# Kernel optimization log

Hardware: AMD Instinct MI355X
Metric: run time of the kernel (lower is better)

Reference implementation:

```python
import jax, jax.numpy as jnp
import numpy as np
import math

FEATURE_DIM = 512
QK_DIM = 256
EPS = 1e-12  # torch F.normalize eps


def _l2norm(x):
    n = jnp.linalg.norm(x, axis=-1, keepdims=True)
    return x / jnp.maximum(n, EPS)


def setup_inputs() -> dict:
    key = jax.random.key(0)
    ks = jax.random.split(key, 6)
    B, Nq, Nk = 16, 2048, 2048
    query = jax.random.normal(ks[0], (B, Nq, FEATURE_DIM), dtype=jnp.float32)
    key_t = jax.random.normal(ks[1], (B, Nk, FEATURE_DIM // 2), dtype=jnp.float32)
    value = jax.random.normal(ks[2], (B, Nk, FEATURE_DIM // 2), dtype=jnp.float32)
    # weights stored torch-style [out, in], init N(0, sqrt(2/out))
    WQ = jax.random.normal(ks[3], (QK_DIM, FEATURE_DIM), dtype=jnp.float32) * math.sqrt(2.0 / QK_DIM)
    WK = jax.random.normal(ks[4], (QK_DIM, FEATURE_DIM // 2), dtype=jnp.float32) * math.sqrt(2.0 / QK_DIM)
    WV = jax.random.normal(ks[5], (FEATURE_DIM, FEATURE_DIM // 2), dtype=jnp.float32) * math.sqrt(2.0 / FEATURE_DIM)
    return {"query": query, "key": key_t, "value": value, "WQ": WQ, "WK": WK, "WV": WV}


def reference(query, key, value, WQ, WK, WV):
    temp = QK_DIM ** (-0.5)
    w_q = _l2norm(jnp.einsum('bnf,qf->bnq', query, WQ))      # [B, Nq, D]
    w_k = _l2norm(jnp.einsum('bmf,qf->bmq', key, WK))        # [B, Nk, D]
    dot = jnp.einsum('bnd,bmd->bnm', w_q, w_k)               # cosine sims
    affinity = jax.nn.softmax(dot * temp, axis=-1)
    w_v = _l2norm(jnp.einsum('bmf,vf->bmv', value, WV))      # [B, Nk, F]
    out = jnp.einsum('bnm,bmv->bnv', affinity, w_v)
    return out + query
```

## Files before the change

### kernel.cpp

```cpp
#include <hip/hip_runtime.h>

typedef float        f32x4  __attribute__((ext_vector_type(4)));
typedef float        f32x16 __attribute__((ext_vector_type(16)));
typedef unsigned int u32x4  __attribute__((ext_vector_type(4)));
typedef unsigned int u32x2  __attribute__((ext_vector_type(2)));
typedef int          i32x2  __attribute__((ext_vector_type(2)));
typedef __bf16       bf16x8 __attribute__((ext_vector_type(8)));

#define DEVFN static __device__ __forceinline__

DEVFN unsigned cvtpk(float a, float b){
  unsigned r;
  asm("v_cvt_pk_bf16_f32 %0, %1, %2" : "=v"(r) : "v"(a), "v"(b));
  return r;
}
DEVFN float exp2_hw(float x){
  float r;
  asm("v_exp_f32 %0, %1" : "=v"(r) : "v"(x));
  return r;
}
DEVFN bf16x8 as_bf(u32x4 v){ union{u32x4 u; bf16x8 b;} x; x.u=v; return x.b; }

DEVFN unsigned char f2fp8(float v){
  int r = __builtin_amdgcn_cvt_pk_fp8_f32(v, v, 0, false);
  return (unsigned char)(r & 0xff);
}
DEVFN unsigned pk4_fp8(float a, float b, float c, float d){
  int r = __builtin_amdgcn_cvt_pk_fp8_f32(a, b, 0, false);
  r = __builtin_amdgcn_cvt_pk_fp8_f32(c, d, r, true);
  return (unsigned)r;
}
DEVFN long mk64(unsigned lo, unsigned hi){
  return (long)(((unsigned long long)hi << 32) | lo);
}

DEVFN void plswap(unsigned &x, unsigned &y, int h){
#if __has_builtin(__builtin_amdgcn_permlane32_swap)
  i32x2 r = __builtin_amdgcn_permlane32_swap((int)x, (int)y, false, false);
  x = (unsigned)r[0]; y = (unsigned)r[1];
#else
  unsigned ox = (unsigned)__shfl_xor((int)x, 32);
  unsigned oy = (unsigned)__shfl_xor((int)y, 32);
  unsigned nx = h ? oy : x;
  unsigned ny = h ? y  : ox;
  x = nx; y = ny;
#endif
}

DEVFN void gload16(const char* src, char* lds){
  __builtin_amdgcn_global_load_lds(
      (__attribute__((address_space(1))) void*)src,
      (__attribute__((address_space(3))) void*)lds, 16, 0, 0);
}

constexpr int BB = 16, NQ = 2048, NK = 2048, F = 512, D = 256, FV = 512;

template<int KD, int ND, int MODE>
__global__ __launch_bounds__(256,2) void proj_kernel(const float* __restrict__ X,
                                                     const float* __restrict__ W,
                                                     unsigned char* __restrict__ Y,
                                                     float scale)
{
  constexpr bool TR = (MODE == 2);
  constexpr int NW = ND/4;
  constexpr int AF = TR ? 8 : 2;
  constexpr int BF = TR ? 2 : NW/16;
  __shared__ __align__(16) char xsm[32*80];
  __shared__ __align__(16) char wsm[ND*80];
  __shared__ float wsum[4][32];
  const int tid = threadIdx.x;
  const int lane = tid & 63;
  const int wid = tid >> 6;
  const int q16 = lane & 15;
  const int g = lane >> 4;
  const int row0 = blockIdx.x * 32;
  const int rX = tid >> 3, cX = (tid & 7) * 4;

  f32x4 z4 = {0.f,0.f,0.f,0.f};
  f32x4 acc[AF][BF];
  #pragma unroll
  for (int i=0;i<AF;i++){
    #pragma unroll
    for (int j=0;j<BF;j++) acc[i][j] = z4;
  }

  for (int k0 = 0; k0 < KD; k0 += 32){
    {
      f32x4 v = *(const f32x4*)(X + (size_t)(row0+rX)*KD + k0 + cX);
      u32x2 p; p[0]=cvtpk(v[0],v[1]); p[1]=cvtpk(v[2],v[3]);
      *(u32x2*)(xsm + rX*80 + cX*2) = p;
    }
    #pragma unroll
    for (int j=0;j<ND/32;j++){
      int r = j*32 + rX;
      f32x4 v = *(const f32x4*)(W + (size_t)r*KD + k0 + cX);
      u32x2 p; p[0]=cvtpk(v[0],v[1]); p[1]=cvtpk(v[2],v[3]);
      *(u32x2*)(wsm + r*80 + cX*2) = p;
    }
    __syncthreads();
    if constexpr (!TR){
      bf16x8 a[2], bb[BF];
      #pragma unroll
      for (int mi=0;mi<2;mi++)  a[mi]  = as_bf(*(const u32x4*)(xsm + (16*mi+q16)*80 + g*16));
      #pragma unroll
      for (int ni=0;ni<BF;ni++) bb[ni] = as_bf(*(const u32x4*)(wsm + (wid*NW + 16*ni + q16)*80 + g*16));
      #pragma unroll
      for (int mi=0;mi<2;mi++){
        #pragma unroll
        for (int ni=0;ni<BF;ni++)
          acc[mi][ni] = __builtin_amdgcn_mfma_f32_16x16x32_bf16(a[mi], bb[ni], acc[mi][ni], 0,0,0);
      }
    } else {
      bf16x8 a[8], bb[2];
      #pragma unroll
      for (int ai=0;ai<8;ai++) a[ai] = as_bf(*(const u32x4*)(wsm + (wid*NW + 16*ai + q16)*80 + g*16));
      #pragma unroll
      for (int ci=0;ci<2;ci++) bb[ci] = as_bf(*(const u32x4*)(xsm + (16*ci+q16)*80 + g*16));
      #pragma unroll
      for (int ai=0;ai<8;ai++){
        #pragma unroll
        for (int ci=0;ci<2;ci++)
          acc[ai][ci] = __builtin_amdgcn_mfma_f32_16x16x32_bf16(a[ai], bb[ci], acc[ai][ci], 0,0,0);
      }
    }
    __syncthreads();
  }

  if constexpr (!TR){
    float part[2][4];
    #pragma unroll
    for (int mi=0;mi<2;mi++){
      #pragma unroll
      for (int r=0;r<4;r++){
        float s=0.f;
        #pragma unroll
        for (int ni=0;ni<BF;ni++){ float v=acc[mi][ni][r]; s += v*v; }
        part[mi][r]=s;
      }
    }
    #pragma unroll
    for (int m=1;m<16;m<<=1){
      #pragma unroll
      for (int mi=0;mi<2;mi++){
        #pragma unroll
        for (int r=0;r<4;r++) part[mi][r] += __shfl_xor(part[mi][r], m);
      }
    }
    if (q16 == 0){
      #pragma unroll
      for (int mi=0;mi<2;mi++){
        #pragma unroll
        for (int r=0;r<4;r++) wsum[wid][16*mi + 4*g + r] = part[mi][r];
      }
    }
    __syncthreads();
    #pragma unroll
    for (int mi=0;mi<2;mi++){
      #pragma unroll
      for (int r=0;r<4;r++){
        int m = 16*mi + 4*g + r;
        float tot = wsum[0][m]+wsum[1][m]+wsum[2][m]+wsum[3][m];
        float inv = scale / fmaxf(sqrtf(tot), 1e-12f);
        int row = row0 + m;
        #pragma unroll
        for (int ni=0;ni<BF;ni++){
          int col = wid*NW + 16*ni + q16;
          unsigned char vb = f2fp8(acc[mi][ni][r]*inv);
          if constexpr (MODE == 0){
            Y[(size_t)row*ND + col] = vb;
          } else {
            int b2 = row >> 11, kv = row & 2047;
            int kt = kv >> 5, mm = kv & 31;
            int u = col >> 5, dd = col & 31;
            int s = ((dd>>4)<<3) | (dd&7);
            int l = mm + ((dd>>3)&1)*32;
            Y[((((size_t)b2*64 + kt)*8 + u)*64 + l)*16 + s] = vb;
          }
        }
      }
    }
  } else {
    float pp[2];
    #pragma unroll
    for (int ci=0;ci<2;ci++){
      float s=0.f;
      #pragma unroll
      for (int ai=0;ai<8;ai++){
        #pragma unroll
        for (int r=0;r<4;r++){ float v=acc[ai][ci][r]; s += v*v; }
      }
      pp[ci]=s;
    }
    #pragma unroll
    for (int ci=0;ci<2;ci++){
      pp[ci] += __shfl_xor(pp[ci],16);
      pp[ci] += __shfl_xor(pp[ci],32);
    }
    if (lane < 16){ wsum[wid][lane] = pp[0]; wsum[wid][16+lane] = pp[1]; }
    __syncthreads();
    #pragma unroll
    for (int ci=0;ci<2;ci++){
      int m = 16*ci + q16;
      float tot = wsum[0][m]+wsum[1][m]+wsum[2][m]+wsum[3][m];
      float inv = scale / fmaxf(sqrtf(tot), 1e-12f);
      int grow = row0 + m;
      int b2 = grow >> 11;
      int kv = grow & 2047;
      int kt = kv >> 5, kl = kv & 31;
      int s = ((kl>>4)<<3) | (kl&7);
      int lofs = ((kl>>3)&1)*32;
      #pragma unroll
      for (int ai=0;ai<8;ai++){
        #pragma unroll
        for (int r=0;r<4;r++){
          int n = wid*NW + 16*ai + 4*g + r;
          int fvh = n >> 8, u = (n>>5)&7, mm = n & 31;
          unsigned char vb = f2fp8(acc[ai][ci][r]*inv);
          Y[(((((size_t)b2*64 + kt)*2 + fvh)*8 + u)*64 + (mm + lofs))*16 + s] = vb;
        }
      }
    }
  }
}

__global__ __launch_bounds__(512,2) void attn_kernel(const float* __restrict__ query,
    const unsigned char* __restrict__ wq8, const unsigned char* __restrict__ k8,
    const unsigned char* __restrict__ v8, float* __restrict__ out)
{
  __shared__ __align__(16) char smem[65536];
  const int tid = threadIdx.x, lane = tid & 63, wid = tid >> 6;
  const int l31 = lane & 31, h = lane >> 5;
  const int qs = wid & 3, fvh = wid >> 2;
  const int bid = blockIdx.x;
  const int lb = (bid & 7)*32 + (bid >> 3);
  const int b = lb >> 4;
  const int qblk = lb & 15;
  const int q0 = qblk*128;

  const char* ksrc = (const char*)(k8 + (size_t)b*524288) + lane*16;
  const char* vsrc = (const char*)(v8 + (size_t)b*1048576) + lane*16;

  #define STAGE(T, CUR) do{                                                       \
    gload16(ksrc + (size_t)(T)*8192  + wid*1024,                                  \
            smem + (CUR)*8192 + wid*1024);                                        \
    gload16(vsrc + (size_t)(T)*16384 + (2*wid  )*1024,                            \
            smem + 16384 + (CUR)*16384 + (2*wid  )*1024);                         \
    gload16(vsrc + (size_t)(T)*16384 + (2*wid+1)*1024,                            \
            smem + 16384 + (CUR)*16384 + (2*wid+1)*1024);                         \
  }while(0)

  STAGE(0, 0);

  unsigned long long qf[16];
  {
    const unsigned char* qb = wq8 + ((size_t)b*NQ + q0 + qs*32 + l31)*D;
    #pragma unroll
    for (int c=0;c<16;c++) qf[c] = *(const unsigned long long*)(qb + c*16 + h*8);
  }

  f32x16 z16;
  #pragma unroll
  for (int i=0;i<16;i++) z16[i]=0.f;
  f32x16 o[8];
  #pragma unroll
  for (int i=0;i<8;i++) o[i]=z16;
  float ssum = 0.f;
  const float c2 = 0.0625f * 1.4426950408889634f / 64.0f;

  __syncthreads();

  #define BODY(T, CUR) do{                                                          \
    if ((T) < 63) STAGE((T)+1, (CUR)^1);                                            \
    const char* kb = smem + (CUR)*8192;                                             \
    const char* vb = smem + 16384 + (CUR)*16384;                                    \
    f32x16 S = z16;                                                                 \
    __builtin_amdgcn_s_setprio(1);                                                  \
    _Pragma("unroll")                                                               \
    for (int u=0;u<8;u++){                                                          \
      u32x4 kk = *(const u32x4*)(kb + u*1024 + lane*16);                            \
      S = __builtin_amdgcn_mfma_f32_32x32x16_fp8_fp8(mk64(kk[0],kk[1]),             \
            (long)qf[2*u],   S, 0,0,0);                                             \
      S = __builtin_amdgcn_mfma_f32_32x32x16_fp8_fp8(mk64(kk[2],kk[3]),             \
            (long)qf[2*u+1], S, 0,0,0);                                             \
    }                                                                               \
    __builtin_amdgcn_s_setprio(0);                                                  \
    float p[16];                                                                    \
    _Pragma("unroll")                                                               \
    for (int r=0;r<16;r++) p[r] = exp2_hw(S[r]*c2);                                 \
    float s2[8];                                                                    \
    _Pragma("unroll")                                                               \
    for (int j=0;j<8;j++) s2[j] = p[2*j] + p[2*j+1];                                \
    float s4a = (s2[0]+s2[1]) + (s2[2]+s2[3]);                                      \
    float s4b = (s2[4]+s2[5]) + (s2[6]+s2[7]);                                      \
    ssum += s4a + s4b;                                                              \
    unsigned d0 = pk4_fp8(p[0],p[1],p[2],p[3]);                   \
    unsigned d1 = pk4_fp8(p[4],p[5],p[6],p[7]);                   \
    unsigned d2 = pk4_fp8(p[8],p[9],p[10],p[11]);                 \
    unsigned d3 = pk4_fp8(p[12],p[13],p[14],p[15]);               \
    plswap(d0, d1, h);  plswap(d2, d3, h);                                          \
    long P0 = mk64(d0, d1);                               \
    long P1 = mk64(d2, d3);                               \
    __builtin_amdgcn_s_setprio(1);                                                  \
    _Pragma("unroll")                                                               \
    for (int u=0;u<8;u++){                                                          \
      u32x4 vv = *(const u32x4*)(vb + (fvh*8+u)*1024 + lane*16);                    \
      o[u] = __builtin_amdgcn_mfma_f32_32x32x16_fp8_fp8(mk64(vv[0],vv[1]), P0,      \
                                                        o[u], 0,0,0);               \
      o[u] = __builtin_amdgcn_mfma_f32_32x32x16_fp8_fp8(mk64(vv[2],vv[3]), P1,      \
                                                        o[u], 0,0,0);               \
    }                                                                               \
    __builtin_amdgcn_s_setprio(0);                                                  \
    __syncthreads();                                                                \
  }while(0)

  for (int tt = 0; tt < 64; tt += 2){
    BODY(tt,   0);
    BODY(tt+1, 1);
  }
  #undef BODY
  #undef STAGE

  ssum += __shfl_xor(ssum, 32);
  const float inv = 1.f/(8.f*ssum);
  #pragma unroll
  for (int i=0;i<8;i++){
    #pragma unroll
    for (int r=0;r<16;r++) o[i][r] *= inv;
  }

  char* wsc = smem + qs*16384;
  union U16 { f32x16 v; f32x4 q4[4]; };
  const int swz = (l31 & 7) << 4;
  #pragma unroll
  for (int phase=0; phase<2; ++phase){
    if (fvh == phase){
      #pragma unroll
      for (int hf=0; hf<2; ++hf){
        #pragma unroll
        for (int fc2=0; fc2<4; ++fc2){
          U16 u; u.v = o[hf*4+fc2];
          #pragma unroll
          for (int k=0;k<4;k++){
            *(f32x4*)(wsc + l31*512 + ((fc2*128 + k*32 + h*16) ^ swz)) = u.q4[k];
          }
        }
        #pragma unroll
        for (int p2=0;p2<16;p2++){
          int qr = p2*2 + h;
          f32x4 v = *(const f32x4*)(wsc + qr*512 + ((l31*16) ^ ((qr&7)<<4)));
          size_t row = (size_t)b*NQ + q0 + qs*32 + qr;
          int col = fvh*256 + hf*128 + l31*4;
          f32x4 qv = *(const f32x4*)(query + row*F + col);
          #pragma unroll
          for (int e=0;e<4;e++) v[e] += qv[e];
          *(f32x4*)(out + row*F + col) = v;
        }
      }
    }
    __syncthreads();
  }
}

extern "C" void kernel_launch(void* const* d_in, const int* in_sizes, int n_in,
                              void* d_out, int out_size, void* d_ws, size_t ws_size,
                              hipStream_t stream)
{
  const float* query = (const float*)d_in[0];
  const float* key   = (const float*)d_in[1];
  const float* value = (const float*)d_in[2];
  const float* WQ    = (const float*)d_in[3];
  const float* WK    = (const float*)d_in[4];
  const float* WV    = (const float*)d_in[5];
  float* out = (float*)d_out;

  unsigned char* wq8 = (unsigned char*)d_ws;
  unsigned char* k8  = wq8 + (size_t)BB*NQ*D;
  unsigned char* v8  = k8  + (size_t)BB*NK*D;

  dim3 blk(256);
  proj_kernel<512,256,0><<<1024, blk, 0, stream>>>(query, WQ, wq8, 8.0f);
  proj_kernel<256,256,1><<<1024, blk, 0, stream>>>(key,   WK, k8,  8.0f);
  proj_kernel<256,512,2><<<1024, blk, 0, stream>>>(value, WV, v8,  8.0f);
  attn_kernel<<<256, dim3(512), 0, stream>>>(query, wq8, k8, v8, out);
}
```

Measured before the change: 195.7 us.

## Prefetch projection tiles into registers and halve attention block size

The projection kernel now loads the next K-slice of X and W into registers before the barrier and MFMA work, so global load latency overlaps compute (register double-buffering). The attention kernel changes from 512-thread blocks covering 128 queries to 256-thread blocks covering 64 queries. The grid doubles to 512 blocks, and the staging loop now issues more loads per thread. This aims at better CU fill and latency hiding, but each K/V tile is now fetched by twice as many blocks, and the extra prefetch registers may cost occupancy.

Result: faster. 189.2 us (-3.3%).

```diff
diff --git a/kernel.cpp b/kernel.cpp
--- a/kernel.cpp
+++ b/kernel.cpp
@@ -84,18 +84,27 @@
     for (int j=0;j<BF;j++) acc[i][j] = z4;
   }
 
+  f32x4 xr = *(const f32x4*)(X + (size_t)(row0+rX)*KD + cX);
+  f32x4 wr[ND/32];
+  #pragma unroll
+  for (int j=0;j<ND/32;j++)
+    wr[j] = *(const f32x4*)(W + (size_t)(j*32+rX)*KD + cX);
+
   for (int k0 = 0; k0 < KD; k0 += 32){
     {
-      f32x4 v = *(const f32x4*)(X + (size_t)(row0+rX)*KD + k0 + cX);
-      u32x2 p; p[0]=cvtpk(v[0],v[1]); p[1]=cvtpk(v[2],v[3]);
+      u32x2 p; p[0]=cvtpk(xr[0],xr[1]); p[1]=cvtpk(xr[2],xr[3]);
       *(u32x2*)(xsm + rX*80 + cX*2) = p;
     }
     #pragma unroll
     for (int j=0;j<ND/32;j++){
-      int r = j*32 + rX;
-      f32x4 v = *(const f32x4*)(W + (size_t)r*KD + k0 + cX);
-      u32x2 p; p[0]=cvtpk(v[0],v[1]); p[1]=cvtpk(v[2],v[3]);
-      *(u32x2*)(wsm + r*80 + cX*2) = p;
+      u32x2 p; p[0]=cvtpk(wr[j][0],wr[j][1]); p[1]=cvtpk(wr[j][2],wr[j][3]);
+      *(u32x2*)(wsm + (j*32+rX)*80 + cX*2) = p;
+    }
+    if (k0 + 32 < KD){
+      xr = *(const f32x4*)(X + (size_t)(row0+rX)*KD + k0+32 + cX);
+      #pragma unroll
+      for (int j=0;j<ND/32;j++)
+        wr[j] = *(const f32x4*)(W + (size_t)(j*32+rX)*KD + k0+32 + cX);
     }
     __syncthreads();
     if constexpr (!TR){
@@ -223,30 +232,36 @@
   }
 }
 
-__global__ __launch_bounds__(512,2) void attn_kernel(const float* __restrict__ query,
+__global__ __launch_bounds__(256,2) void attn_kernel(const float* __restrict__ query,
     const unsigned char* __restrict__ wq8, const unsigned char* __restrict__ k8,
     const unsigned char* __restrict__ v8, float* __restrict__ out)
 {
   __shared__ __align__(16) char smem[65536];
   const int tid = threadIdx.x, lane = tid & 63, wid = tid >> 6;
   const int l31 = lane & 31, h = lane >> 5;
-  const int qs = wid & 3, fvh = wid >> 2;
+  const int qs = wid & 1, fvh = wid >> 1;
   const int bid = blockIdx.x;
-  const int lb = (bid & 7)*32 + (bid >> 3);
-  const int b = lb >> 4;
-  const int qblk = lb & 15;
-  const int q0 = qblk*128;
-
-  const char* ksrc = (const char*)(k8 + (size_t)b*524288) + lane*16;
+  const int lb = (bid & 7)*64 + (bid >> 3);
+  const int b = lb >> 5;
+  const int qblk = lb & 31;
+  const int q0 = qblk*64;
+
+  const char* ksrc = (const char*)(k8 + (size_t)b*524288)  + lane*16;
   const char* vsrc = (const char*)(v8 + (size_t)b*1048576) + lane*16;
 
   #define STAGE(T, CUR) do{                                                       \
-    gload16(ksrc + (size_t)(T)*8192  + wid*1024,                                  \
-            smem + (CUR)*8192 + wid*1024);                                        \
-    gload16(vsrc + (size_t)(T)*16384 + (2*wid  )*1024,                            \
-            smem + 16384 + (CUR)*16384 + (2*wid  )*1024);                         \
-    gload16(vsrc + (size_t)(T)*16384 + (2*wid+1)*1024,                            \
-            smem + 16384 + (CUR)*16384 + (2*wid+1)*1024);                         \
+    gload16(ksrc + (size_t)(T)*8192  +        wid*1024,                           \
+            smem + (CUR)*8192 +        wid*1024);                                 \
+    gload16(ksrc + (size_t)(T)*8192  + 4096 + wid*1024,                           \
+            smem + (CUR)*8192 + 4096 + wid*1024);                                 \
+    gload16(vsrc + (size_t)(T)*16384 +         wid*1024,                          \
+            smem + 16384 + (CUR)*16384 +         wid*1024);                       \
+    gload16(vsrc + (size_t)(T)*16384 +  4096 + wid*1024,                          \
+            smem + 16384 + (CUR)*16384 +  4096 + wid*1024);                       \
+    gload16(vsrc + (size_t)(T)*16384 +  8192 + wid*1024,                          \
+            smem + 16384 + (CUR)*16384 +  8192 + wid*1024);                       \
+    gload16(vsrc + (size_t)(T)*16384 + 12288 + wid*1024,                          \
+            smem + 16384 + (CUR)*16384 + 12288 + wid*1024);                       \
   }while(0)
 
   STAGE(0, 0);
@@ -381,5 +396,5 @@
   proj_kernel<512,256,0><<<1024, blk, 0, stream>>>(query, WQ, wq8, 8.0f);
   proj_kernel<256,256,1><<<1024, blk, 0, stream>>>(key,   WK, k8,  8.0f);
   proj_kernel<256,512,2><<<1024, blk, 0, stream>>>(value, WV, v8,  8.0f);
-  attn_kernel<<<256, dim3(512), 0, stream>>>(query, wq8, k8, v8, out);
-}
+  attn_kernel<<<512, blk, 0, stream>>>(query, wq8, k8, v8, out);
+}
```
